# Optimization experiments

Measured on AMD Instinct MI355X. Metric: run time of the kernel, lower is better.

Reference implementation:

```python
import jax, jax.numpy as jnp
import numpy as np

B, N, F = 8, 1024, 256
OUT, REL = 256, 16
NADJ = 7  # ((2 relations + consecutive) * 2 for backward) + self link


def setup_inputs() -> dict:
    key = jax.random.key(0)
    k0, k1, k2, k3, k4 = jax.random.split(key, 5)
    features = jax.random.normal(k0, (B, N, F), dtype=jnp.float32)
    A1 = jax.random.uniform(k1, (B, N, N), dtype=jnp.float32)
    A2 = jax.random.uniform(k2, (B, N, N), dtype=jnp.float32)
    # learned params: one (F+REL, OUT) weight per adjacency matrix, edge embeddings init 'ones', bias (N, OUT)
    W = jax.random.normal(k3, (NADJ, F + REL, OUT), dtype=jnp.float32) * 0.05
    W_edges = jnp.ones((NADJ, REL), dtype=jnp.float32)
    b = jax.random.uniform(k4, (N, OUT), dtype=jnp.float32, minval=-0.05, maxval=0.05)
    return {"features": features, "A1": A1, "A2": A2, "W": W, "W_edges": W_edges, "b": b}


def reference(features, A1, A2, W, W_edges, b):
    # eye = A[0] * zeros(N) + eye(N)  -> batch-broadcast identity [B,N,N]
    eye = jnp.zeros_like(A1) + jnp.eye(N, dtype=A1.dtype)
    # original rolls along axis 0 (batch) of the broadcast identity (faithful replication)
    shifted = jnp.roll(eye, 1, axis=0)
    A_fwd = [A1, A2, shifted]                      # relations + consecutive link
    A_list = A_fwd + [jnp.swapaxes(a, 1, 2) for a in A_fwd]  # backward links
    A_list.append(eye)                             # self links
    A = jnp.stack(A_list, axis=0)                  # [R,B,N,N]

    # concat(features, tile(W_edges[r])) @ W[r] == features @ W[r][:F] + W_edges[r] @ W[r][F:]
    HW = jnp.einsum('bnf,rfo->rbno', features, W[:, :F]) \
         + jnp.einsum('rd,rdo->ro', W_edges, W[:, F:])[:, None, None, :]  # [R,B,N,OUT]
    AHW = jnp.einsum('rbnm,rbmo->rbno', A, HW)     # batched adjacency matmul
    out = jnp.max(AHW, axis=0) + b                 # max-aggregate over relations, add bias
    return out                                     # activation = linear
```

## Files before the change

### kernel.cpp

```cpp
#include <hip/hip_runtime.h>
#include <hip/hip_bf16.h>

#define B_ 8
#define N_ 1024
#define F_ 256
#define OUT_ 256
#define REL_ 16
#define NADJ_ 7

typedef __attribute__((ext_vector_type(8))) _Float16 f16x8;
typedef __attribute__((ext_vector_type(4))) _Float16 f16x4;
typedef __attribute__((ext_vector_type(4))) float f32x4;

__device__ __forceinline__ void gll16(const _Float16* g, _Float16* l) {
    __builtin_amdgcn_global_load_lds(
        (const __attribute__((address_space(1))) void*)g,
        (__attribute__((address_space(3))) void*)l, 16, 0, 0);
}

__device__ __forceinline__ f16x8 cvt8(float4 a, float4 b) {
    return f16x8{(_Float16)a.x, (_Float16)a.y, (_Float16)a.z, (_Float16)a.w,
                 (_Float16)b.x, (_Float16)b.y, (_Float16)b.z, (_Float16)b.w};
}

#define MEMPIN() asm volatile("" ::: "memory")

__constant__ const int c_perm[7] = {0, 1, 3, 4, 2, 5, 6};

__global__ __launch_bounds__(256) void prep_kernel(const float* __restrict__ W,
                                                   const float* __restrict__ We,
                                                   const float* __restrict__ feat,
                                                   float* __restrict__ cb,
                                                   _Float16* __restrict__ WTp,
                                                   _Float16* __restrict__ Fe) {
    int bid = blockIdx.x, tid = threadIdx.x;
    if (bid < 7) {
        int idx = bid * 256 + tid;
        int j = idx / OUT_, o = idx % OUT_;
        int r = c_perm[j];
        const float* Wr = W + (size_t)r * (F_ + REL_) * OUT_;
        float s = 0.f;
#pragma unroll
        for (int d = 0; d < REL_; ++d) s += We[r * REL_ + d] * Wr[(F_ + d) * OUT_ + o];
        cb[idx] = s;
    } else if (bid < 1799) {
        int idx = (bid - 7) * 256 + tid;
        int j = idx >> 16, rem = idx & 65535, o = rem >> 8, f = rem & 255;
        int r = c_perm[j];
        WTp[idx] = (_Float16)W[((size_t)r * (F_ + REL_) + f) * OUT_ + o];
    } else {
        int i = (bid - 1799) * 256 + tid;
        size_t base = (size_t)i * 8;
        float4 a = *(const float4*)(feat + base);
        float4 b = *(const float4*)(feat + base + 4);
        *(f16x8*)(Fe + base) = cvt8(a, b);
    }
}

__global__ __launch_bounds__(256) void hw7_kernel(const _Float16* __restrict__ Fe,
                                                  const _Float16* __restrict__ WTp,
                                                  const float* __restrict__ cb,
                                                  _Float16* __restrict__ HWT,
                                                  _Float16* __restrict__ HWN) {
    __shared__ _Float16 S[3 * 8192];
    const int bid = blockIdx.x, tid = threadIdx.x;
    const int z = bid / 128, rem = bid % 128, bx = rem & 63, by = rem >> 6;
    const bool tr = (z < 4);
    const _Float16* A  = tr ? (WTp + (size_t)z * 65536) : Fe;
    const _Float16* Bt = tr ? Fe : (WTp + (size_t)z * 65536);
    const int m0 = (tr ? by : bx) * 128;
    const int n0 = (tr ? bx : by) * 128;
    const int wave = tid >> 6, lane = tid & 63, lm = lane & 15, q = lane >> 4;
    const int wr = (wave >> 1) * 64, wc = (wave & 1) * 64;
    const int srow = tid >> 2, sk = (tid & 3) * 8;
    const _Float16* ga0 = A + (size_t)(m0 + srow) * F_ + sk;
    const _Float16* ga1 = ga0 + (size_t)64 * F_;
    const _Float16* gb0 = Bt + (size_t)(n0 + srow) * F_ + sk;
    const _Float16* gb1 = gb0 + (size_t)64 * F_;

    f32x4 acc[4][4] = {};
    const int NT = 8;

    {
        gll16(ga0, S + tid * 8);
        gll16(ga1, S + 2048 + tid * 8);
        gll16(gb0, S + 4096 + tid * 8);
        gll16(gb1, S + 6144 + tid * 8);
        MEMPIN();
        gll16(ga0 + 32, S + 8192 + tid * 8);
        gll16(ga1 + 32, S + 8192 + 2048 + tid * 8);
        gll16(gb0 + 32, S + 8192 + 4096 + tid * 8);
        gll16(gb1 + 32, S + 8192 + 6144 + tid * 8);
        asm volatile("s_waitcnt vmcnt(4)" ::: "memory");
        __builtin_amdgcn_s_barrier();
    }
    int cs = 0, ns = 1, fs = 2;
    for (int t = 0; t < NT; ++t) {
        if (t + 2 < NT) {
            const int k = (t + 2) * 32;
            _Float16* sb = S + fs * 8192;
            gll16(ga0 + k, sb + tid * 8);
            gll16(ga1 + k, sb + 2048 + tid * 8);
            gll16(gb0 + k, sb + 4096 + tid * 8);
            gll16(gb1 + k, sb + 6144 + tid * 8);
        }
        {
            const _Float16* Au = S + cs * 8192;
            const _Float16* Bu = Au + 4096;
            f16x8 af[4], bf[4];
#pragma unroll
            for (int i = 0; i < 4; ++i) af[i] = *(const f16x8*)(Au + (wr + i * 16 + lm) * 32 + q * 8);
#pragma unroll
            for (int j = 0; j < 4; ++j) bf[j] = *(const f16x8*)(Bu + (wc + j * 16 + lm) * 32 + q * 8);
            __builtin_amdgcn_s_setprio(1);
#pragma unroll
            for (int i = 0; i < 4; ++i)
#pragma unroll
                for (int j = 0; j < 4; ++j)
                    acc[i][j] = __builtin_amdgcn_mfma_f32_16x16x32_f16(af[i], bf[j], acc[i][j], 0, 0, 0);
            __builtin_amdgcn_s_setprio(0);
        }
        if (t + 1 < NT) {
            if (t + 2 < NT) asm volatile("s_waitcnt vmcnt(4)" ::: "memory");
            else            asm volatile("s_waitcnt vmcnt(0)" ::: "memory");
            __builtin_amdgcn_s_barrier();
        }
        int tmp = cs; cs = ns; ns = fs; fs = tmp;
    }
    const float* cbz = cb + (size_t)z * 256;
    if (tr) {
        _Float16* C = HWT + (size_t)z * (8 * 256 * 1024) + (size_t)(n0 >> 10) * (256 * 1024);
        const int nl = n0 & 1023;
#pragma unroll
        for (int i = 0; i < 4; ++i)
#pragma unroll
            for (int j = 0; j < 4; ++j)
#pragma unroll
                for (int g = 0; g < 4; ++g) {
                    int row = wr + i * 16 + q * 4 + g;
                    int col = wc + j * 16 + lm;
                    float v = acc[i][j][g] + cbz[m0 + row];
                    C[(size_t)(m0 + row) * 1024 + nl + col] = (_Float16)v;
                }
    } else {
        _Float16* C = HWN + (size_t)(z - 4) * ((size_t)8192 * 256);
#pragma unroll
        for (int i = 0; i < 4; ++i)
#pragma unroll
            for (int j = 0; j < 4; ++j)
#pragma unroll
                for (int g = 0; g < 4; ++g) {
                    int row = wr + i * 16 + q * 4 + g;
                    int col = wc + j * 16 + lm;
                    float v = acc[i][j][g] + cbz[n0 + col];
                    C[(size_t)(m0 + row) * 256 + (n0 + col)] = (_Float16)v;
                }
    }
}

__global__ __launch_bounds__(256) void p2_kernel(const float* __restrict__ A1,
                                                 const float* __restrict__ A2,
                                                 const _Float16* __restrict__ HWT,
                                                 _Float16* __restrict__ AHW) {
    __shared__ _Float16 As[2 * 8192];
    __shared__ _Float16 Bs[2 * 8192];
    const int d = blockIdx.x;
    const int xcd = d & 7, slot = d >> 3;
    const int Ghi = xcd + 8 * (slot >> 4);
    const int member = (slot >> 3) & 1;
    const int mt = slot & 7;
    const int kh = Ghi & 1;
    const int zz = Ghi >> 1;
    const int rr = zz >> 3, b = zz & 7;

    const size_t slab = (size_t)B_ * N_ * OUT_;
    const _Float16* Bt = HWT + (size_t)(rr * 8 + b) * (256 * 1024);
    _Float16* C = AHW + (size_t)kh * (4 * slab) + (size_t)rr * slab + (size_t)b * (N_ * OUT_);
    const int m0 = mt * 128, n0 = member * 128, kbase = kh * 512;
    const int tid = threadIdx.x;
    const int wave = tid >> 6, lane = tid & 63, lm = lane & 15, q = lane >> 4;
    const int wr = (wave >> 1) * 64, wc = (wave & 1) * 64;
    const int srow = tid >> 2, sk = (tid & 3) * 8;
    const _Float16* gb0 = Bt + (size_t)(n0 + srow) * 1024 + kbase + sk;
    const _Float16* gb1 = gb0 + (size_t)64 * 1024;

    const float* Ag = ((rr & 1) ? A2 : A1) + (size_t)b * N_ * N_;
    f32x4 acc[4][4] = {};

    auto domfma = [&](int buf) {
#pragma unroll
        for (int u2 = 0; u2 < 2; ++u2) {
            const _Float16* Au = As + buf * 8192 + u2 * 4096;
            const _Float16* Bu = Bs + buf * 8192 + u2 * 4096;
            f16x8 af[4], bf[4];
#pragma unroll
            for (int i = 0; i < 4; ++i)
                af[i] = *(const f16x8*)(Au + (wr + i * 16 + lm) * 32 + ((q ^ i) * 8));
#pragma unroll
            for (int j = 0; j < 4; ++j)
                bf[j] = *(const f16x8*)(Bu + (wc + j * 16 + lm) * 32 + q * 8);
            __builtin_amdgcn_s_setprio(1);
#pragma unroll
            for (int i = 0; i < 4; ++i)
#pragma unroll
                for (int j = 0; j < 4; ++j)
                    acc[i][j] = __builtin_amdgcn_mfma_f32_16x16x32_f16(af[i], bf[j], acc[i][j], 0, 0, 0);
            __builtin_amdgcn_s_setprio(0);
        }
    };

    auto stageB = [&](int buf, int k2) {
        _Float16* base = Bs + buf * 8192;
        gll16(gb0 + k2,      base + tid * 8);
        gll16(gb0 + k2 + 32, base + 4096 + tid * 8);
        gll16(gb1 + k2,      base + 2048 + tid * 8);
        gll16(gb1 + k2 + 32, base + 6144 + tid * 8);
    };

    if (rr < 2) {
        const float* Ag0 = Ag + (size_t)(m0 + srow) * N_ + kbase + sk;
        const float* Ag1 = Ag0 + (size_t)64 * N_;
        const int sx = ((tid & 3) ^ ((tid >> 6) & 3)) * 8;
        float4 r0a, r0b, r1a, r1b, r2a, r2b, r3a, r3b;
        auto RDA = [&](int k2) {
            r0a = *(const float4*)(Ag0 + k2);      r0b = *(const float4*)(Ag0 + k2 + 4);
            r1a = *(const float4*)(Ag0 + k2 + 32); r1b = *(const float4*)(Ag0 + k2 + 36);
            r2a = *(const float4*)(Ag1 + k2);      r2b = *(const float4*)(Ag1 + k2 + 4);
            r3a = *(const float4*)(Ag1 + k2 + 32); r3b = *(const float4*)(Ag1 + k2 + 36);
        };
        auto WRA = [&](int buf) {
            _Float16* la = As + buf * 8192 + srow * 32 + sx;
            *(f16x8*)(la)        = cvt8(r0a, r0b);
            *(f16x8*)(la + 4096) = cvt8(r1a, r1b);
            *(f16x8*)(la + 2048) = cvt8(r2a, r2b);
            *(f16x8*)(la + 6144) = cvt8(r3a, r3b);
        };
        RDA(0);
        WRA(0);
        stageB(0, 0);
        RDA(64);
        __syncthreads();
        for (int t = 0; t < 8; ++t) {
            const int cur = t & 1, nxt = cur ^ 1;
            if (t < 7) {
                WRA(nxt);
                stageB(nxt, (t + 1) * 64);
                if (t < 6) RDA((t + 2) * 64);
            }
            domfma(cur);
            __syncthreads();
        }
    } else {
        const int kk4 = (tid >> 4) * 4;
        const int ms = (tid & 15) * 8;
        const int u = kk4 >> 5, kl = kk4 & 31;
        const int tsw = ((ms >> 4) & 3) << 3;
        const int wof = u * 4096 + ms * 32 + (kl ^ tsw);
        const float* gA = Ag + (size_t)(kbase + kk4) * N_ + m0 + ms;
        float4 ra0, rb0, ra1, rb1, ra2, rb2, ra3, rb3;
        auto RDT = [&](int t) {
            const float* p = gA + (size_t)t * 64 * N_;
            ra0 = *(const float4*)(p);            rb0 = *(const float4*)(p + 4);
            ra1 = *(const float4*)(p + N_);       rb1 = *(const float4*)(p + N_ + 4);
            ra2 = *(const float4*)(p + 2 * N_);   rb2 = *(const float4*)(p + 2 * N_ + 4);
            ra3 = *(const float4*)(p + 3 * N_);   rb3 = *(const float4*)(p + 3 * N_ + 4);
        };
        auto WRT = [&](int buf) {
            _Float16* wp = As + buf * 8192 + wof;
            *(f16x4*)(wp + 0 * 32) = f16x4{(_Float16)ra0.x, (_Float16)ra1.x, (_Float16)ra2.x, (_Float16)ra3.x};
            *(f16x4*)(wp + 1 * 32) = f16x4{(_Float16)ra0.y, (_Float16)ra1.y, (_Float16)ra2.y, (_Float16)ra3.y};
            *(f16x4*)(wp + 2 * 32) = f16x4{(_Float16)ra0.z, (_Float16)ra1.z, (_Float16)ra2.z, (_Float16)ra3.z};
            *(f16x4*)(wp + 3 * 32) = f16x4{(_Float16)ra0.w, (_Float16)ra1.w, (_Float16)ra2.w, (_Float16)ra3.w};
            *(f16x4*)(wp + 4 * 32) = f16x4{(_Float16)rb0.x, (_Float16)rb1.x, (_Float16)rb2.x, (_Float16)rb3.x};
            *(f16x4*)(wp + 5 * 32) = f16x4{(_Float16)rb0.y, (_Float16)rb1.y, (_Float16)rb2.y, (_Float16)rb3.y};
            *(f16x4*)(wp + 6 * 32) = f16x4{(_Float16)rb0.z, (_Float16)rb1.z, (_Float16)rb2.z, (_Float16)rb3.z};
            *(f16x4*)(wp + 7 * 32) = f16x4{(_Float16)rb0.w, (_Float16)rb1.w, (_Float16)rb2.w, (_Float16)rb3.w};
        };
        RDT(0);
        WRT(0);
        stageB(0, 0);
        RDT(1);
        __syncthreads();
        for (int t = 0; t < 8; ++t) {
            const int cur = t & 1, nxt = cur ^ 1;
            if (t < 7) {
                WRT(nxt);
                stageB(nxt, (t + 1) * 64);
                if (t < 6) RDT(t + 2);
            }
            domfma(cur);
            __syncthreads();
        }
    }
#pragma unroll
    for (int i = 0; i < 4; ++i)
#pragma unroll
        for (int j = 0; j < 4; ++j)
#pragma unroll
            for (int g = 0; g < 4; ++g) {
                int row = wr + i * 16 + q * 4 + g;
                int col = wc + j * 16 + lm;
                C[(size_t)(m0 + row) * 256 + (n0 + col)] = (_Float16)acc[i][j][g];
            }
}

__global__ __launch_bounds__(256) void max_kernel(const _Float16* __restrict__ AHW,
                                                  const _Float16* __restrict__ HWN,
                                                  const float* __restrict__ bias,
                                                  float* __restrict__ out) {
    size_t i = ((size_t)blockIdx.x * 256 + threadIdx.x) * 8;
    const size_t slab = (size_t)B_ * N_ * OUT_;
    const size_t HS = 4 * slab;
    float m[8];
    {
        f16x8 v0 = *(const f16x8*)(AHW + i);
        f16x8 v1 = *(const f16x8*)(AHW + HS + i);
#pragma unroll
        for (int e = 0; e < 8; ++e) m[e] = (float)v0[e] + (float)v1[e];
    }
#pragma unroll
    for (int rr = 1; rr < 4; ++rr) {
        f16x8 v0 = *(const f16x8*)(AHW + rr * slab + i);
        f16x8 v1 = *(const f16x8*)(AHW + HS + rr * slab + i);
#pragma unroll
        for (int e = 0; e < 8; ++e) m[e] = fmaxf(m[e], (float)v0[e] + (float)v1[e]);
    }
#pragma unroll
    for (int j = 0; j < 3; ++j) {
        f16x8 w = *(const f16x8*)(HWN + j * slab + i);
#pragma unroll
        for (int e = 0; e < 8; ++e) m[e] = fmaxf(m[e], (float)w[e]);
    }
    size_t bidx = i & ((size_t)N_ * OUT_ - 1);
    float4 b0 = *(const float4*)(bias + bidx);
    float4 b1 = *(const float4*)(bias + bidx + 4);
    float4 o0 = {m[0] + b0.x, m[1] + b0.y, m[2] + b0.z, m[3] + b0.w};
    float4 o1 = {m[4] + b1.x, m[5] + b1.y, m[6] + b1.z, m[7] + b1.w};
    *(float4*)(out + i) = o0;
    *(float4*)(out + i + 4) = o1;
}

__global__ void cbias_kernel(const float* __restrict__ W, const float* __restrict__ We,
                             float* __restrict__ c) {
    int idx = blockIdx.x * 256 + threadIdx.x;
    if (idx >= NADJ_ * OUT_) return;
    int r = idx / OUT_, o = idx % OUT_;
    const float* Wr = W + (size_t)r * (F_ + REL_) * OUT_;
    float s = 0.f;
#pragma unroll
    for (int d = 0; d < REL_; ++d) s += We[r * REL_ + d] * Wr[(F_ + d) * OUT_ + o];
    c[idx] = s;
}

__global__ __launch_bounds__(256) void hw_kernel(const float* __restrict__ feat,
                                                 const float* __restrict__ W,
                                                 const float* __restrict__ cb,
                                                 _Float16* __restrict__ HWb) {
    __shared__ _Float16 As[64][32];
    __shared__ _Float16 Bs[64][32];
    const int mt = blockIdx.x, ct = blockIdx.y;
    const int tid = threadIdx.x, wave = tid >> 6, lane = tid & 63;
    const int r = (ct * 64) / OUT_;
    const int o0 = (ct * 64) % OUT_;
    const float* Bg = W + (size_t)r * (F_ + REL_) * OUT_ + o0;
    const int m0 = mt * 64;
    const int lm = lane & 15, q = lane >> 4;
    f32x4 acc[4] = {};
    for (int k0 = 0; k0 < F_; k0 += 32) {
        {
            int seg = (tid & 3) * 8, m = tid >> 2;
            const float* src = feat + (size_t)(m0 + m) * F_ + k0 + seg;
#pragma unroll
            for (int j = 0; j < 8; ++j) As[m][seg + j] = (_Float16)src[j];
        }
        {
            int kk = tid >> 3, ns = (tid & 7) * 8;
            const float* src = Bg + (size_t)(k0 + kk) * OUT_ + ns;
#pragma unroll
            for (int j = 0; j < 8; ++j) Bs[ns + j][kk] = (_Float16)src[j];
        }
        __syncthreads();
        f16x8 a = *(const f16x8*)&As[wave * 16 + lm][q * 8];
#pragma unroll
        for (int c4 = 0; c4 < 4; ++c4) {
            f16x8 b = *(const f16x8*)&Bs[c4 * 16 + lm][q * 8];
            acc[c4] = __builtin_amdgcn_mfma_f32_16x16x32_f16(a, b, acc[c4], 0, 0, 0);
        }
        __syncthreads();
    }
#pragma unroll
    for (int c4 = 0; c4 < 4; ++c4)
#pragma unroll
        for (int g = 0; g < 4; ++g) {
            int row = wave * 16 + (lane >> 4) * 4 + g;
            int col = c4 * 16 + lm;
            float v = acc[c4][g] + cb[r * OUT_ + o0 + col];
            HWb[((size_t)r * B_ * N_ + m0 + row) * OUT_ + o0 + col] = (_Float16)v;
        }
}

__global__ __launch_bounds__(256) void agg_kernel(const float* __restrict__ A1,
                                                  const float* __restrict__ A2,
                                                  const _Float16* __restrict__ HWb,
                                                  const float* __restrict__ bias,
                                                  float* __restrict__ out) {
    __shared__ _Float16 As[64][32];
    __shared__ _Float16 Bs[64][32];
    const int b = blockIdx.z, nt = blockIdx.y, ot = blockIdx.x;
    const int tid = threadIdx.x, wave = tid >> 6, lane = tid & 63;
    const int n0 = nt * 64, o0 = ot * 64;
    const int lm = lane & 15, q = lane >> 4;
    const size_t rstride = (size_t)B_ * N_ * OUT_;
    f32x4 mx[4];
#pragma unroll
    for (int i = 0; i < 4; ++i) mx[i] = f32x4{-1e30f, -1e30f, -1e30f, -1e30f};
#pragma unroll 1
    for (int rr = 0; rr < 4; ++rr) {
        const float* Ag = ((rr & 1) ? A2 : A1) + (size_t)b * N_ * N_;
        const bool tr = (rr >= 2);
        const int r = (rr < 2) ? rr : rr + 1;
        const _Float16* Bg = HWb + (size_t)r * rstride + (size_t)b * N_ * OUT_ + o0;
        f32x4 acc[4] = {};
        for (int k0 = 0; k0 < N_; k0 += 32) {
            if (!tr) {
                int seg = (tid & 3) * 8, m = tid >> 2;
                const float* src = Ag + (size_t)(n0 + m) * N_ + k0 + seg;
#pragma unroll
                for (int j = 0; j < 8; ++j) As[m][seg + j] = (_Float16)src[j];
            } else {
                int kk = tid >> 3, ms = (tid & 7) * 8;
                const float* src = Ag + (size_t)(k0 + kk) * N_ + n0 + ms;
#pragma unroll
                for (int j = 0; j < 8; ++j) As[ms + j][kk] = (_Float16)src[j];
            }
            {
                int kk = tid >> 3, ns = (tid & 7) * 8;
                const _Float16* src = Bg + (size_t)(k0 + kk) * OUT_ + ns;
#pragma unroll
                for (int j = 0; j < 8; ++j) Bs[ns + j][kk] = src[j];
            }
            __syncthreads();
            f16x8 a = *(const f16x8*)&As[wave * 16 + lm][q * 8];
#pragma unroll
            for (int c4 = 0; c4 < 4; ++c4) {
                f16x8 bb = *(const f16x8*)&Bs[c4 * 16 + lm][q * 8];
                acc[c4] = __builtin_amdgcn_mfma_f32_16x16x32_f16(a, bb, acc[c4], 0, 0, 0);
            }
            __syncthreads();
        }
#pragma unroll
        for (int c4 = 0; c4 < 4; ++c4)
#pragma unroll
            for (int g = 0; g < 4; ++g) mx[c4][g] = fmaxf(mx[c4][g], acc[c4][g]);
    }
#pragma unroll
    for (int c4 = 0; c4 < 4; ++c4)
#pragma unroll
        for (int g = 0; g < 4; ++g) {
            int row = wave * 16 + (lane >> 4) * 4 + g;
            int col = c4 * 16 + lm;
            size_t pos = ((size_t)b * N_ + n0 + row) * OUT_ + o0 + col;
            float v = mx[c4][g];
            v = fmaxf(v, (float)HWb[2 * rstride + pos]);
            v = fmaxf(v, (float)HWb[5 * rstride + pos]);
            v = fmaxf(v, (float)HWb[6 * rstride + pos]);
            out[pos] = v + bias[((size_t)(n0 + row)) * OUT_ + o0 + col];
        }
}

extern "C" void kernel_launch(void* const* d_in, const int* in_sizes, int n_in,
                              void* d_out, int out_size, void* d_ws, size_t ws_size,
                              hipStream_t stream) {
    const float* feat = (const float*)d_in[0];
    const float* A1   = (const float*)d_in[1];
    const float* A2   = (const float*)d_in[2];
    const float* W    = (const float*)d_in[3];
    const float* We   = (const float*)d_in[4];
    const float* bias = (const float*)d_in[5];
    float* out = (float*)d_out;

    const size_t OFF_CB   = 0;
    const size_t OFF_WT   = 8192;
    const size_t OFF_FE   = 1048576;
    const size_t OFF_HWT  = 5242880;
    const size_t OFF_HWN  = 22020096;
    const size_t OFF_AHW  = 34603008;
    const size_t WS_NEEDED = 68157440;

    if (ws_size >= WS_NEEDED) {
        float*    cbp = (float*)((char*)d_ws + OFF_CB);
        _Float16* WTp = (_Float16*)((char*)d_ws + OFF_WT);
        _Float16* Fe  = (_Float16*)((char*)d_ws + OFF_FE);
        _Float16* HWT = (_Float16*)((char*)d_ws + OFF_HWT);
        _Float16* HWN = (_Float16*)((char*)d_ws + OFF_HWN);
        _Float16* AHW = (_Float16*)((char*)d_ws + OFF_AHW);

        prep_kernel<<<2823, 256, 0, stream>>>(W, We, feat, cbp, WTp, Fe);
        hw7_kernel<<<896, 256, 0, stream>>>(Fe, WTp, cbp, HWT, HWN);
        p2_kernel<<<1024, 256, 0, stream>>>(A1, A2, HWT, AHW);
        max_kernel<<<1024, 256, 0, stream>>>(AHW, HWN, bias, out);
    } else {
        float* cb = (float*)d_ws;
        _Float16* HWb = (_Float16*)((char*)d_ws + 8192);
        cbias_kernel<<<7, 256, 0, stream>>>(W, We, cb);
        hw_kernel<<<dim3(128, 28), 256, 0, stream>>>(feat, W, cb, HWb);
        agg_kernel<<<dim3(4, 16, 8), 256, 0, stream>>>(A1, A2, HWb, bias, out);
    }
}
```

Measured before the change: 167.5 us.

## Deepen A-operand register prefetch to two stages with explicit vmcnt barriers

Both A-loading paths now keep two register staging sets, so the fp32 adjacency tiles are fetched three iterations ahead instead of two. The __syncthreads calls are replaced with manual s_waitcnt vmcnt/lgkmcnt plus s_barrier and sched_barrier, letting outstanding global loads stay in flight across the barrier. The goal is to hide more global memory latency behind the MFMA work. In exchange it uses more registers, which may lower occupancy, and the hand-set vmcnt counts must match the exact number of issued loads, including the global_load_lds B stages.

```diff
diff --git a/kernel.cpp b/kernel.cpp
--- a/kernel.cpp
+++ b/kernel.cpp
@@ -221,34 +221,45 @@
         const float* Ag0 = Ag + (size_t)(m0 + srow) * N_ + kbase + sk;
         const float* Ag1 = Ag0 + (size_t)64 * N_;
         const int sx = ((tid & 3) ^ ((tid >> 6) & 3)) * 8;
-        float4 r0a, r0b, r1a, r1b, r2a, r2b, r3a, r3b;
-        auto RDA = [&](int k2) {
-            r0a = *(const float4*)(Ag0 + k2);      r0b = *(const float4*)(Ag0 + k2 + 4);
-            r1a = *(const float4*)(Ag0 + k2 + 32); r1b = *(const float4*)(Ag0 + k2 + 36);
-            r2a = *(const float4*)(Ag1 + k2);      r2b = *(const float4*)(Ag1 + k2 + 4);
-            r3a = *(const float4*)(Ag1 + k2 + 32); r3b = *(const float4*)(Ag1 + k2 + 36);
+        float4 P[2][8];
+        auto RDA = [&](int s, int k2) {
+            P[s][0] = *(const float4*)(Ag0 + k2);      P[s][1] = *(const float4*)(Ag0 + k2 + 4);
+            P[s][2] = *(const float4*)(Ag0 + k2 + 32); P[s][3] = *(const float4*)(Ag0 + k2 + 36);
+            P[s][4] = *(const float4*)(Ag1 + k2);      P[s][5] = *(const float4*)(Ag1 + k2 + 4);
+            P[s][6] = *(const float4*)(Ag1 + k2 + 32); P[s][7] = *(const float4*)(Ag1 + k2 + 36);
         };
-        auto WRA = [&](int buf) {
+        auto WRA = [&](int s, int buf) {
             _Float16* la = As + buf * 8192 + srow * 32 + sx;
-            *(f16x8*)(la)        = cvt8(r0a, r0b);
-            *(f16x8*)(la + 4096) = cvt8(r1a, r1b);
-            *(f16x8*)(la + 2048) = cvt8(r2a, r2b);
-            *(f16x8*)(la + 6144) = cvt8(r3a, r3b);
+            *(f16x8*)(la)        = cvt8(P[s][0], P[s][1]);
+            *(f16x8*)(la + 4096) = cvt8(P[s][2], P[s][3]);
+            *(f16x8*)(la + 2048) = cvt8(P[s][4], P[s][5]);
+            *(f16x8*)(la + 6144) = cvt8(P[s][6], P[s][7]);
         };
-        RDA(0);
-        WRA(0);
         stageB(0, 0);
-        RDA(64);
-        __syncthreads();
+        RDA(0, 0);
+        WRA(0, 0);
+        RDA(0, 64);
+        RDA(1, 128);
+        asm volatile("s_waitcnt vmcnt(16)" ::: "memory");
+        asm volatile("s_waitcnt lgkmcnt(0)" ::: "memory");
+        __builtin_amdgcn_s_barrier();
+        __builtin_amdgcn_sched_barrier(0);
+#pragma unroll
         for (int t = 0; t < 8; ++t) {
             const int cur = t & 1, nxt = cur ^ 1;
             if (t < 7) {
-                WRA(nxt);
                 stageB(nxt, (t + 1) * 64);
-                if (t < 6) RDA((t + 2) * 64);
-            }
+                WRA(t & 1, nxt);
+            }
+            if (t < 5) RDA(t & 1, (t + 3) * 64);
             domfma(cur);
-            __syncthreads();
+            if (t < 7) {
+                if (t < 5) asm volatile("s_waitcnt vmcnt(8)" ::: "memory");
+                else       asm volatile("s_waitcnt vmcnt(0)" ::: "memory");
+                asm volatile("s_waitcnt lgkmcnt(0)" ::: "memory");
+                __builtin_amdgcn_s_barrier();
+                __builtin_amdgcn_sched_barrier(0);
+            }
         }
     } else {
         const int kk4 = (tid >> 4) * 4;
@@ -257,39 +268,50 @@
         const int tsw = ((ms >> 4) & 3) << 3;
         const int wof = u * 4096 + ms * 32 + (kl ^ tsw);
         const float* gA = Ag + (size_t)(kbase + kk4) * N_ + m0 + ms;
-        float4 ra0, rb0, ra1, rb1, ra2, rb2, ra3, rb3;
-        auto RDT = [&](int t) {
+        f32x4 R[2][8];
+        auto RDT = [&](int s, int t) {
             const float* p = gA + (size_t)t * 64 * N_;
-            ra0 = *(const float4*)(p);            rb0 = *(const float4*)(p + 4);
-            ra1 = *(const float4*)(p + N_);       rb1 = *(const float4*)(p + N_ + 4);
-            ra2 = *(const float4*)(p + 2 * N_);   rb2 = *(const float4*)(p + 2 * N_ + 4);
-            ra3 = *(const float4*)(p + 3 * N_);   rb3 = *(const float4*)(p + 3 * N_ + 4);
+            R[s][0] = *(const f32x4*)(p);            R[s][1] = *(const f32x4*)(p + 4);
+            R[s][2] = *(const f32x4*)(p + N_);       R[s][3] = *(const f32x4*)(p + N_ + 4);
+            R[s][4] = *(const f32x4*)(p + 2 * N_);   R[s][5] = *(const f32x4*)(p + 2 * N_ + 4);
+            R[s][6] = *(const f32x4*)(p + 3 * N_);   R[s][7] = *(const f32x4*)(p + 3 * N_ + 4);
         };
-        auto WRT = [&](int buf) {
+        auto WRT = [&](int s, int buf) {
             _Float16* wp = As + buf * 8192 + wof;
-            *(f16x4*)(wp + 0 * 32) = f16x4{(_Float16)ra0.x, (_Float16)ra1.x, (_Float16)ra2.x, (_Float16)ra3.x};
-            *(f16x4*)(wp + 1 * 32) = f16x4{(_Float16)ra0.y, (_Float16)ra1.y, (_Float16)ra2.y, (_Float16)ra3.y};
-            *(f16x4*)(wp + 2 * 32) = f16x4{(_Float16)ra0.z, (_Float16)ra1.z, (_Float16)ra2.z, (_Float16)ra3.z};
-            *(f16x4*)(wp + 3 * 32) = f16x4{(_Float16)ra0.w, (_Float16)ra1.w, (_Float16)ra2.w, (_Float16)ra3.w};
-            *(f16x4*)(wp + 4 * 32) = f16x4{(_Float16)rb0.x, (_Float16)rb1.x, (_Float16)rb2.x, (_Float16)rb3.x};
-            *(f16x4*)(wp + 5 * 32) = f16x4{(_Float16)rb0.y, (_Float16)rb1.y, (_Float16)rb2.y, (_Float16)rb3.y};
-            *(f16x4*)(wp + 6 * 32) = f16x4{(_Float16)rb0.z, (_Float16)rb1.z, (_Float16)rb2.z, (_Float16)rb3.z};
-            *(f16x4*)(wp + 7 * 32) = f16x4{(_Float16)rb0.w, (_Float16)rb1.w, (_Float16)rb2.w, (_Float16)rb3.w};
+#pragma unroll
+            for (int c = 0; c < 4; ++c)
+                *(f16x4*)(wp + c * 32) = f16x4{(_Float16)R[s][0][c], (_Float16)R[s][2][c],
+                                               (_Float16)R[s][4][c], (_Float16)R[s][6][c]};
+#pragma unroll
+            for (int c = 0; c < 4; ++c)
+                *(f16x4*)(wp + (4 + c) * 32) = f16x4{(_Float16)R[s][1][c], (_Float16)R[s][3][c],
+                                                     (_Float16)R[s][5][c], (_Float16)R[s][7][c]};
         };
-        RDT(0);
-        WRT(0);
         stageB(0, 0);
-        RDT(1);
-        __syncthreads();
+        RDT(0, 0);
+        WRT(0, 0);
+        RDT(0, 1);
+        RDT(1, 2);
+        asm volatile("s_waitcnt vmcnt(16)" ::: "memory");
+        asm volatile("s_waitcnt lgkmcnt(0)" ::: "memory");
+        __builtin_amdgcn_s_barrier();
+        __builtin_amdgcn_sched_barrier(0);
+#pragma unroll
         for (int t = 0; t < 8; ++t) {
             const int cur = t & 1, nxt = cur ^ 1;
             if (t < 7) {
-                WRT(nxt);
                 stageB(nxt, (t + 1) * 64);
-                if (t < 6) RDT(t + 2);
-            }
+                WRT(t & 1, nxt);
+            }
+            if (t < 5) RDT(t & 1, t + 3);
             domfma(cur);
-            __syncthreads();
+            if (t < 7) {
+                if (t < 5) asm volatile("s_waitcnt vmcnt(8)" ::: "memory");
+                else       asm volatile("s_waitcnt vmcnt(0)" ::: "memory");
+                asm volatile("s_waitcnt lgkmcnt(0)" ::: "memory");
+                __builtin_amdgcn_s_barrier();
+                __builtin_amdgcn_sched_barrier(0);
+            }
         }
     }
 #pragma unroll
```

Measured after the change: 170.1 us. About the same (+1.6%).
